# Performance work log

Measured on AMD Instinct MI355X. Metric: run time of the kernel, lower is better.

## Reference

```python
import jax, jax.numpy as jnp
import numpy as np

B, N, DEPTH = 64, 196, 6
EMBED = 384; CDIM = 384; DIM = EMBED + CDIM            # 768
HEADS = 8; DH = 64; INNER = HEADS * DH                 # 512
VD = INNER + CDIM; DV = VD // HEADS                    # 896, 112
SCALE = DH ** -0.5
EPS = 1e-5


def _bn(x, g, b):
    # BatchNorm1d in training mode applied to (b, e, n): per-channel stats over (b, n)
    m = x.mean(axis=(0, 1))
    v = x.var(axis=(0, 1))  # biased variance, as torch BN uses for normalization
    return (x - m) * jax.lax.rsqrt(v + EPS) * g + b


def setup_inputs() -> dict:
    key = jax.random.key(0)
    ks = jax.random.split(key, 8)
    s = 0.02
    d = {}
    d["x"] = jax.random.normal(ks[0], (B, N, DIM), jnp.float32)
    d["bn1_g"] = jnp.ones((DEPTH, DIM), jnp.float32)
    d["bn1_b"] = jnp.zeros((DEPTH, DIM), jnp.float32)
    d["Wqk"] = jax.random.normal(ks[1], (DEPTH, EMBED, 2 * INNER), jnp.float32) * s
    d["bqk"] = jnp.zeros((DEPTH, 2 * INNER), jnp.float32)
    d["Wv"] = jax.random.normal(ks[2], (DEPTH, DIM, VD), jnp.float32) * s
    d["bv"] = jnp.zeros((DEPTH, VD), jnp.float32)
    d["Wo"] = jax.random.normal(ks[3], (DEPTH, VD, DIM), jnp.float32) * s
    d["bo"] = jnp.zeros((DEPTH, DIM), jnp.float32)
    d["bn2_g"] = jnp.ones((DEPTH, DIM), jnp.float32)
    d["bn2_b"] = jnp.zeros((DEPTH, DIM), jnp.float32)
    d["W1"] = jax.random.normal(ks[4], (DEPTH, DIM, DIM), jnp.float32) * s
    d["b1"] = jnp.zeros((DEPTH, DIM), jnp.float32)
    d["bn3_g"] = jnp.ones((DEPTH, DIM), jnp.float32)
    d["bn3_b"] = jnp.zeros((DEPTH, DIM), jnp.float32)
    d["W2"] = jax.random.normal(ks[5], (DEPTH, DIM, DIM), jnp.float32) * s
    d["b2"] = jnp.zeros((DEPTH, DIM), jnp.float32)
    return d


def reference(x, bn1_g, bn1_b, Wqk, bqk, Wv, bv, Wo, bo,
              bn2_g, bn2_b, W1, b1, bn3_g, bn3_b, W2, b2):
    for i in range(DEPTH):
        # PreNorm(BatchNorm) + Attention + residual
        h = _bn(x, bn1_g[i], bn1_b[i])
        qk = h[:, :, -CDIM:] @ Wqk[i] + bqk[i]          # (B,N,2*INNER) from class slice
        q, k = jnp.split(qk, 2, axis=-1)
        v = h @ Wv[i] + bv[i]                            # (B,N,VD) from full dim
        q = q.reshape(B, N, HEADS, DH).transpose(0, 2, 1, 3)   # b h n d
        k = k.reshape(B, N, HEADS, DH).transpose(0, 2, 1, 3)
        v = v.reshape(B, N, HEADS, DV).transpose(0, 2, 1, 3)
        attn = jax.nn.softmax(jnp.einsum('bhnd,bhmd->bhnm', q, k) * SCALE, axis=-1)
        o = jnp.einsum('bhnm,bhmd->bhnd', attn, v)
        o = o.transpose(0, 2, 1, 3).reshape(B, N, VD)
        x = x + (o @ Wo[i] + bo[i])
        # PreNorm(BatchNorm) + FeedForward (Linear -> BN -> GELU -> Linear) + residual
        h = _bn(x, bn2_g[i], bn2_b[i])
        f = _bn(h @ W1[i] + b1[i], bn3_g[i], bn3_b[i])
        f = jax.nn.gelu(f, approximate=False)            # torch nn.GELU default (exact)
        x = x + (f @ W2[i] + b2[i])
    return x
```

## Files before the change

### kernel.cpp

```cpp
#include <hip/hip_runtime.h>
#include <hip/hip_bf16.h>
#include <stdint.h>


typedef __bf16 bf16x8 __attribute__((ext_vector_type(8)));
typedef __bf16 bf16x4 __attribute__((ext_vector_type(4)));
typedef float  f32x4  __attribute__((ext_vector_type(4)));

#define DIM_  768
#define SCALE_ 0.125f

__device__ __forceinline__ void gload16(const void* g, void* l) {
  __builtin_amdgcn_global_load_lds(
      (__attribute__((address_space(1))) void*)(g),
      (__attribute__((address_space(3))) void*)(l), 16, 0, 0);
}

__device__ __forceinline__ uint32_t cvt_pk_bf16(float lo, float hi) {
  uint32_t r;
  asm("v_cvt_pk_bf16_f32 %0, %1, %2" : "=v"(r) : "v"(lo), "v"(hi));
  return r;
}

__global__ void transpose_cvt(const float* __restrict__ W, __bf16* __restrict__ WT,
                              int K, int N) {
  __shared__ float t[32][33];
  const size_t zoff = (size_t)blockIdx.z * K * N;
  W  += zoff; WT += zoff;
  const int bx = blockIdx.x * 32;
  const int by = blockIdx.y * 32;
  for (int j = threadIdx.y; j < 32; j += 8)
    t[j][threadIdx.x] = W[(size_t)(by + j) * N + bx + threadIdx.x];
  __syncthreads();
  for (int j = threadIdx.y; j < 32; j += 8)
    WT[(size_t)(bx + j) * K + by + threadIdx.x] = (__bf16)t[threadIdx.x][j];
}

__global__ void cvt_bf16(const float* __restrict__ src, __bf16* __restrict__ dst) {
  const int i = blockIdx.x * 256 + threadIdx.x;
  f32x4 v = *(const f32x4*)(src + (size_t)i * 4);
  bf16x4 o;
  o[0] = (__bf16)v[0]; o[1] = (__bf16)v[1]; o[2] = (__bf16)v[2]; o[3] = (__bf16)v[3];
  *(bf16x4*)(dst + (size_t)i * 4) = o;
}

__global__ void bn_stats_part(const float* __restrict__ x, float* __restrict__ part) {
  const int col = blockIdx.x * 256 + threadIdx.x;
  const int r0  = blockIdx.y * 64;
  const float* p = x + (size_t)r0 * DIM_ + col;
  float s = 0.f, s2 = 0.f;
  for (int r = 0; r < 64; ++r) {
    float v = p[(size_t)r * DIM_];
    s += v; s2 += v * v;
  }
  float* q = part + ((size_t)blockIdx.y * DIM_ + col) * 2;
  q[0] = s; q[1] = s2;
}

__global__ void bn_stats_fin(const float* __restrict__ part, const float* __restrict__ g,
                             const float* __restrict__ b, float* __restrict__ sc) {
  const int col = blockIdx.x * 256 + threadIdx.x;
  float s = 0.f, s2 = 0.f;
  for (int p = 0; p < 196; ++p) {
    s  += part[((size_t)p * DIM_ + col) * 2];
    s2 += part[((size_t)p * DIM_ + col) * 2 + 1];
  }
  const float mean = s * (1.f / 12544.f);
  const float var  = s2 * (1.f / 12544.f) - mean * mean;
  const float rstd = rsqrtf(var + 1e-5f);
  const float scale = rstd * g[col];
  sc[col]        = scale;
  sc[DIM_ + col] = b[col] - mean * scale;
}

__global__ void bn_fin2(float* __restrict__ acc, const float* __restrict__ g,
                        const float* __restrict__ b, float* __restrict__ sc) {
  const int col = blockIdx.x * 256 + threadIdx.x;
  const float s  = acc[col * 2];
  const float s2 = acc[col * 2 + 1];
  acc[col * 2] = 0.f; acc[col * 2 + 1] = 0.f;
  const float mean = s * (1.f / 12544.f);
  const float var  = s2 * (1.f / 12544.f) - mean * mean;
  const float rstd = rsqrtf(var + 1e-5f);
  const float scale = rstd * g[col];
  sc[col]        = scale;
  sc[DIM_ + col] = b[col] - mean * scale;
}

__global__ void fold_attn(const __bf16* __restrict__ wqkT, const __bf16* __restrict__ wvT,
                          const float* __restrict__ bqk, const float* __restrict__ bv,
                          const float* __restrict__ sc,
                          __bf16* __restrict__ wqkT2, __bf16* __restrict__ wvT2,
                          float* __restrict__ bqk2, float* __restrict__ bv2) {
  const int b = blockIdx.x, tid = threadIdx.x;
  if (b < 192) {
    const int e = b * 2048 + tid * 8;
    const int k0 = e % 384;
    bf16x8 w = *(const bf16x8*)(wqkT + e);
    bf16x8 o;
#pragma unroll
    for (int j = 0; j < 8; ++j) o[j] = (__bf16)((float)w[j] * sc[384 + k0 + j]);
    *(bf16x8*)(wqkT2 + e) = o;
  } else if (b < 528) {
    const int e = (b - 192) * 2048 + tid * 8;
    const int k0 = e % 768;
    bf16x8 w = *(const bf16x8*)(wvT + e);
    bf16x8 o;
#pragma unroll
    for (int j = 0; j < 8; ++j) o[j] = (__bf16)((float)w[j] * sc[k0 + j]);
    *(bf16x8*)(wvT2 + e) = o;
  } else {
    const int lane = tid & 63, wv_ = tid >> 6;
    const int idx = (b - 528) * 4 + wv_;
    float acc = 0.f;
    if (idx < 1024) {
      for (int k = lane; k < 384; k += 64)
        acc += (float)wqkT[(size_t)idx * 384 + k] * sc[1152 + k];
#pragma unroll
      for (int off = 32; off; off >>= 1) acc += __shfl_xor(acc, off);
      if (lane == 0) bqk2[idx] = bqk[idx] + acc;
    } else {
      const int n2 = idx - 1024;
      for (int k = lane; k < 768; k += 64)
        acc += (float)wvT[(size_t)n2 * 768 + k] * sc[768 + k];
#pragma unroll
      for (int off = 32; off; off >>= 1) acc += __shfl_xor(acc, off);
      if (lane == 0) bv2[n2] = bv[n2] + acc;
    }
  }
}

__global__ void fold_ffn(const __bf16* __restrict__ w1T, const float* __restrict__ b1,
                         const float* __restrict__ sc,
                         __bf16* __restrict__ w1T2, float* __restrict__ b12) {
  const int b = blockIdx.x, tid = threadIdx.x;
  if (b < 288) {
    const int e = b * 2048 + tid * 8;
    const int k0 = e % 768;
    bf16x8 w = *(const bf16x8*)(w1T + e);
    bf16x8 o;
#pragma unroll
    for (int j = 0; j < 8; ++j) o[j] = (__bf16)((float)w[j] * sc[k0 + j]);
    *(bf16x8*)(w1T2 + e) = o;
  } else {
    const int lane = tid & 63, wv_ = tid >> 6;
    const int idx = (b - 288) * 4 + wv_;
    float acc = 0.f;
    for (int k = lane; k < 768; k += 64)
      acc += (float)w1T[(size_t)idx * 768 + k] * sc[768 + k];
#pragma unroll
    for (int off = 32; off; off >>= 1) acc += __shfl_xor(acc, off);
    if (lane == 0) b12[idx] = b1[idx] + acc;
  }
}

__global__ void bn_gelu_apply(const __bf16* __restrict__ f1, const float* __restrict__ sc,
                              __bf16* __restrict__ h) {
  const int i = blockIdx.x * 256 + threadIdx.x;
  const int c4 = i % 192;
  bf16x4 v4 = *(const bf16x4*)(f1 + (size_t)i * 4);
  f32x4 scl = *(const f32x4*)(sc + c4 * 4);
  f32x4 sh  = *(const f32x4*)(sc + DIM_ + c4 * 4);
  bf16x4 o;
#pragma unroll
  for (int j = 0; j < 4; ++j) {
    float y = (float)v4[j] * scl[j] + sh[j];
    float gl = 0.5f * y * (1.f + erff(y * 0.70710678118654752f));
    o[j] = (__bf16)gl;
  }
  *(bf16x4*)(h + (size_t)i * 4) = o;
}

template <int EPI, int STATS, int PANEL_X, int FINAL>
__global__ __launch_bounds__(256, 2) void gemm128(
    const __bf16* __restrict__ A, int lda,
    const __bf16* __restrict__ BT, int K,
    const float* __restrict__ bias,
    __bf16* outB, const __bf16* res16, float* __restrict__ outF, int ldc,
    float* __restrict__ statsAcc, int P, int S) {
  __shared__ __bf16 sA[128 * 64];
  __shared__ __bf16 sB[128 * 64];
  const int bid = blockIdx.x;
  const int xcd = bid & 7, r0b = bid >> 3;
  const int pl = r0b / S, sh = r0b - pl * S;
  const int p = pl * 8 + xcd;
  if (p >= P) return;
  const int mx = PANEL_X ? p : sh;
  const int ny = PANEL_X ? sh : p;

  const int tid = threadIdx.x;
  const int lane = tid & 63, wv = tid >> 6;
  const int l15 = lane & 15, hi = lane >> 4;
  const int m0 = mx * 128, n0 = ny * 128;
  const __bf16* Ab = A + (size_t)m0 * lda;
  const __bf16* Bb = BT + (size_t)n0 * K;
  const int wr = (wv >> 1) * 64, wc = (wv & 1) * 64;

  f32x4 acc[4][4] = {};

#define STAGE(kt)                                                             \
  {                                                                           \
    const int k0_ = (kt) << 6;                                                \
    _Pragma("unroll")                                                         \
    for (int i_ = 0; i_ < 4; ++i_) {                                          \
      const int o_ = i_ * 4096 + tid * 16;                                    \
      const int row_ = o_ >> 7;                                               \
      const int j_ = (o_ >> 4) & 7;                                           \
      const int src_ = (j_ ^ (row_ & 7)) << 3;                                \
      gload16(Ab + (size_t)row_ * lda + k0_ + src_,                           \
              &sA[i_ * 2048 + wv * 512]);                                     \
      gload16(Bb + (size_t)row_ * K + k0_ + src_,                             \
              &sB[i_ * 2048 + wv * 512]);                                     \
    }                                                                         \
  }

  const int nkt = K >> 6;
  for (int kt = 0; kt < nkt; ++kt) {
    if (kt) __syncthreads();
    STAGE(kt);
    asm volatile("s_waitcnt vmcnt(0)" ::: "memory");
    __syncthreads();
    const char* cA = (const char*)sA;
    const char* cB = (const char*)sB;
#pragma unroll
    for (int ks = 0; ks < 2; ++ks) {
      bf16x8 af[4], bfr[4];
#pragma unroll
      for (int m = 0; m < 4; ++m) {
        const int row = wr + m * 16 + l15;
        af[m] = *(const bf16x8*)(cA + row * 128 +
                                 ((ks * 64 + hi * 16) ^ ((row & 7) << 4)));
      }
#pragma unroll
      for (int n = 0; n < 4; ++n) {
        const int row = wc + n * 16 + l15;
        bfr[n] = *(const bf16x8*)(cB + row * 128 +
                                  ((ks * 64 + hi * 16) ^ ((row & 7) << 4)));
      }
#pragma unroll
      for (int m = 0; m < 4; ++m)
#pragma unroll
        for (int n = 0; n < 4; ++n)
          acc[m][n] = __builtin_amdgcn_mfma_f32_16x16x32_bf16(af[m], bfr[n], acc[m][n], 0, 0, 0);
    }
  }
#undef STAGE

  float* scol = (float*)sA;
  if (STATS) {
    __syncthreads();
    scol[tid] = 0.f;
    __syncthreads();
  }

  float cs[4], cs2[4];
  if (STATS)
#pragma unroll
    for (int n = 0; n < 4; ++n) { cs[n] = 0.f; cs2[n] = 0.f; }

#pragma unroll
  for (int m = 0; m < 4; ++m)
#pragma unroll
    for (int n = 0; n < 4; ++n) {
      const int cc = n0 + wc + n * 16 + l15;
      const float bc = (EPI == 2) ? 0.f : bias[cc];
      const int bbq = cc / 196, nn = cc - (cc / 196) * 196;
#pragma unroll
      for (int r = 0; r < 4; ++r) {
        const int rr = m0 + wr + m * 16 + hi * 4 + r;
        const float val = acc[m][n][r] + ((EPI == 2) ? bias[rr] : bc);
        float fv;
        if (EPI == 1) {
          const size_t idx = (size_t)rr * ldc + cc;
          fv = (float)res16[idx] + val;
          if (FINAL) outF[idx] = fv;
          else       outB[idx] = (__bf16)fv;
        } else if (EPI == 2) {
          fv = val;
          const int hq = rr / 112, dd = rr - (rr / 112) * 112;
          outB[((size_t)(bbq * 8 + hq) * 112 + dd) * 224 + nn] = (__bf16)fv;
        } else {
          fv = val;
          outB[(size_t)rr * ldc + cc] = (__bf16)fv;
        }
        if (STATS) { cs[n] += fv; cs2[n] += fv * fv; }
      }
    }

  if (STATS) {
#pragma unroll
    for (int n = 0; n < 4; ++n) {
      float s = cs[n], s2 = cs2[n];
      s += __shfl_xor(s, 16); s2 += __shfl_xor(s2, 16);
      s += __shfl_xor(s, 32); s2 += __shfl_xor(s2, 32);
      if (lane < 16) {
        atomicAdd(&scol[(wc + n * 16 + l15) * 2], s);
        atomicAdd(&scol[(wc + n * 16 + l15) * 2 + 1], s2);
      }
    }
    __syncthreads();
    if (tid < 128) {
      atomicAdd(&statsAcc[(size_t)(n0 + tid) * 2], scol[tid * 2]);
      atomicAdd(&statsAcc[(size_t)(n0 + tid) * 2 + 1], scol[tid * 2 + 1]);
    }
  }
}

#define SVOFF 25088
__global__ __launch_bounds__(512, 1) void attn_kernel(
    const __bf16* __restrict__ qk, const __bf16* __restrict__ vT,
    __bf16* __restrict__ og) {
  __shared__ __align__(16) char smem[75264];
  const int bid = blockIdx.x;
  const int half = bid >> 9, pairid = bid & 511;
  const int bb = pairid >> 3, hh = pairid & 7;
  const int tid = threadIdx.x, lane = tid & 63;
  const int wv = tid >> 6;
  const int l15 = lane & 15, hi = lane >> 4;

  const __bf16* qbase = qk + (size_t)bb * (196 * 1024) + hh * 64;
  const __bf16* kbase = qbase + 512;
  const __bf16* vbase = vT + (size_t)(bb * 8 + hh) * (112 * 224);
  __bf16* obase = og + (size_t)bb * (196 * 896) + hh * 112;

  char* sV = smem + SVOFF;

  for (int s = tid; s < 1568; s += 512) {
    const int n = s >> 3, j = s & 7;
    const int k8 = j ^ (n & 7);
    gload16(kbase + (size_t)n * 1024 + k8 * 8, smem + ((s >> 6) << 10));
  }
  for (int s = tid; s < 112 * 28; s += 512) {
    const int d = s / 28, j = s - d * 28;
    gload16(vbase + d * 224 + ((j ^ (d & 3)) << 3), sV + d * 448 + j * 16);
  }
  asm volatile("s_waitcnt vmcnt(0)" ::: "memory");
  __syncthreads();

  const int qt = half * 7 + wv;
  if (wv < 7 && qt < 13) {
    const int q0 = qt * 16;
    int qn = q0 + l15; if (qn > 195) qn = 195;
    const __bf16* qp = qbase + (size_t)qn * 1024 + hi * 8;
    const bf16x8 qa0 = *(const bf16x8*)(qp);
    const bf16x8 qa1 = *(const bf16x8*)(qp + 32);

    f32x4 s[13] = {};
#pragma unroll
    for (int nf = 0; nf < 13; ++nf) {
      int j = nf * 16 + l15; if (j > 195) j = 195;
      const int sw = (j & 7) << 4;
      const bf16x8 kb0 = *(const bf16x8*)(smem + j * 128 + ((hi * 16) ^ sw));
      const bf16x8 kb1 = *(const bf16x8*)(smem + j * 128 + ((64 + hi * 16) ^ sw));
      s[nf] = __builtin_amdgcn_mfma_f32_16x16x32_bf16(kb0, qa0, s[nf], 0, 0, 0);
      s[nf] = __builtin_amdgcn_mfma_f32_16x16x32_bf16(kb1, qa1, s[nf], 0, 0, 0);
    }

    float mx = -3.0e38f;
#pragma unroll
    for (int nf = 0; nf < 12; ++nf)
#pragma unroll
      for (int r = 0; r < 4; ++r) mx = fmaxf(mx, s[nf][r]);
    if (hi == 0)
#pragma unroll
      for (int r = 0; r < 4; ++r) mx = fmaxf(mx, s[12][r]);
    mx = fmaxf(mx, __shfl_xor(mx, 16));
    mx = fmaxf(mx, __shfl_xor(mx, 32));
    float sum = 0.f;
#pragma unroll
    for (int nf = 0; nf < 12; ++nf)
#pragma unroll
      for (int r = 0; r < 4; ++r) {
        const float pv = __expf((s[nf][r] - mx) * SCALE_);
        s[nf][r] = pv; sum += pv;
      }
#pragma unroll
    for (int r = 0; r < 4; ++r) {
      const float pv = (hi == 0) ? __expf((s[12][r] - mx) * SCALE_) : 0.f;
      s[12][r] = pv; sum += pv;
    }
    sum += __shfl_xor(sum, 16);
    sum += __shfl_xor(sum, 32);
    const float inv = 1.f / sum;
#pragma unroll
    for (int nf = 0; nf < 13; ++nf)
#pragma unroll
      for (int r = 0; r < 4; ++r) s[nf][r] *= inv;

    f32x4 oa[7] = {};
    const int sLo = l15 + ((hi & 1) << 5);
    const int sHi = sLo + 16;
    const bool up = (hi >> 1) != 0;
#pragma unroll
    for (int kk = 0; kk < 7; ++kk) {
      const uint32_t a0 = cvt_pk_bf16(s[2 * kk][0], s[2 * kk][1]);
      const uint32_t a1 = cvt_pk_bf16(s[2 * kk][2], s[2 * kk][3]);
      const uint32_t w0a = (uint32_t)__shfl((int)a0, sLo, 64);
      const uint32_t w1a = (uint32_t)__shfl((int)a1, sLo, 64);
      const uint32_t w2a = (uint32_t)__shfl((int)a0, sHi, 64);
      const uint32_t w3a = (uint32_t)__shfl((int)a1, sHi, 64);
      uint32_t w0, w1, w2, w3;
      if (kk < 6) {
        const uint32_t b0 = cvt_pk_bf16(s[2 * kk + 1][0], s[2 * kk + 1][1]);
        const uint32_t b1 = cvt_pk_bf16(s[2 * kk + 1][2], s[2 * kk + 1][3]);
        const uint32_t w0b = (uint32_t)__shfl((int)b0, sLo, 64);
        const uint32_t w1b = (uint32_t)__shfl((int)b1, sLo, 64);
        const uint32_t w2b = (uint32_t)__shfl((int)b0, sHi, 64);
        const uint32_t w3b = (uint32_t)__shfl((int)b1, sHi, 64);
        w0 = up ? w0b : w0a; w1 = up ? w1b : w1a;
        w2 = up ? w2b : w2a; w3 = up ? w3b : w3a;
      } else {
        w0 = up ? 0u : w0a; w1 = up ? 0u : w1a;
        w2 = up ? 0u : w2a; w3 = up ? 0u : w3a;
      }
      union { uint32_t u[4]; bf16x8 v; } pa;
      pa.u[0] = w0; pa.u[1] = w1; pa.u[2] = w2; pa.u[3] = w3;
#pragma unroll
      for (int nf = 0; nf < 7; ++nf) {
        const int d = nf * 16 + l15;
        const bf16x8 vbf = *(const bf16x8*)(sV + d * 448 +
                              ((kk * 64 + hi * 16) ^ ((d & 3) << 4)));
        oa[nf] = __builtin_amdgcn_mfma_f32_16x16x32_bf16(pa.v, vbf, oa[nf], 0, 0, 0);
      }
    }
#pragma unroll
    for (int nf = 0; nf < 7; ++nf)
#pragma unroll
      for (int r = 0; r < 4; ++r) {
        const int q = q0 + hi * 4 + r;
        if (q < 196) obase[(size_t)q * 896 + nf * 16 + l15] = (__bf16)oa[nf][r];
      }
  }
}

extern "C" void kernel_launch(void* const* d_in, const int* in_sizes, int n_in,
                              void* d_out, int out_size, void* d_ws, size_t ws_size,
                              hipStream_t stream) {
  (void)in_sizes; (void)n_in; (void)out_size; (void)ws_size;
  const float* x_in  = (const float*)d_in[0];
  const float* bn1_g = (const float*)d_in[1];
  const float* bn1_b = (const float*)d_in[2];
  const float* Wqk   = (const float*)d_in[3];
  const float* bqk   = (const float*)d_in[4];
  const float* Wv    = (const float*)d_in[5];
  const float* bv    = (const float*)d_in[6];
  const float* Wo    = (const float*)d_in[7];
  const float* bo    = (const float*)d_in[8];
  const float* bn2_g = (const float*)d_in[9];
  const float* bn2_b = (const float*)d_in[10];
  const float* W1    = (const float*)d_in[11];
  const float* b1    = (const float*)d_in[12];
  const float* bn3_g = (const float*)d_in[13];
  const float* bn3_b = (const float*)d_in[14];
  const float* W2    = (const float*)d_in[15];
  const float* b2    = (const float*)d_in[16];

  char* ws = (char*)d_ws;
  __bf16* vTb  = (__bf16*)(ws + 0);
  __bf16* wqkT = (__bf16*)(ws + 38535168);
  __bf16* wvT  = (__bf16*)(ws + 43253760);
  __bf16* woT  = (__bf16*)(ws + 51511296);
  __bf16* w1T  = (__bf16*)(ws + 59768832);
  __bf16* w2T  = (__bf16*)(ws + 66846720);
  __bf16* xb16 = (__bf16*)(ws + 73924608);
  __bf16* qkb  = (__bf16*)(ws + 93192192);
  __bf16* obuf = (__bf16*)(ws + 141361152);
  float*  part = (float*)(ws + 163840000);
  float*  sc   = (float*)(ws + 165044224);
  float*  sAcc = (float*)(ws + 165051392);
  __bf16* wqkT2= (__bf16*)(ws + 165057536);
  __bf16* wvT2 = (__bf16*)(ws + 165843968);
  __bf16* w1T2 = (__bf16*)(ws + 167220224);
  float*  bqk2 = (float*)(ws + 168399872);
  float*  bv2  = (float*)(ws + 168403968);
  float*  b12  = (float*)(ws + 168407552);
  __bf16* f1b  = qkb;
  __bf16* gout = obuf;

  const dim3 tb(256);
  const dim3 tb512(512);

  transpose_cvt<<<dim3(32, 12, 6), dim3(32, 8), 0, stream>>>(Wqk, wqkT, 384, 1024);
  transpose_cvt<<<dim3(28, 24, 6), dim3(32, 8), 0, stream>>>(Wv,  wvT,  768, 896);
  transpose_cvt<<<dim3(24, 28, 6), dim3(32, 8), 0, stream>>>(Wo,  woT,  896, 768);
  transpose_cvt<<<dim3(24, 24, 6), dim3(32, 8), 0, stream>>>(W1,  w1T,  768, 768);
  transpose_cvt<<<dim3(24, 24, 6), dim3(32, 8), 0, stream>>>(W2,  w2T,  768, 768);
  cvt_bf16<<<9408, tb, 0, stream>>>(x_in, xb16);
  hipMemsetAsync(sAcc, 0, 768 * 2 * sizeof(float), stream);
  hipMemsetAsync(vTb, 0, (size_t)512 * 112 * 224 * 2, stream);

  bn_stats_part<<<dim3(3, 196), tb, 0, stream>>>(x_in, part);
  bn_stats_fin<<<3, tb, 0, stream>>>(part, bn1_g, bn1_b, sc);

  const int gQK = 8 * 13 * 8;
  const int gV  = 8 * 13 * 7;
  const int gO  = 8 * 13 * 6;

  for (int i = 0; i < 6; ++i) {
    const __bf16* wqkT_i = wqkT + (size_t)i * 1024 * 384;
    const __bf16* wvT_i  = wvT  + (size_t)i * 896 * 768;
    const __bf16* woT_i  = woT  + (size_t)i * 768 * 896;
    const __bf16* w1T_i  = w1T  + (size_t)i * 768 * 768;
    const __bf16* w2T_i  = w2T  + (size_t)i * 768 * 768;

    fold_attn<<<1008, tb, 0, stream>>>(wqkT_i, wvT_i, bqk + i * 1024, bv + i * 896,
                                       sc, wqkT2, wvT2, bqk2, bv2);
    gemm128<0, 0, 1, 0><<<gQK, tb, 0, stream>>>(xb16 + 384, 768, wqkT2, 384,
                                                bqk2, qkb, nullptr, nullptr, 1024,
                                                nullptr, 98, 8);
    gemm128<2, 0, 0, 0><<<gV, tb, 0, stream>>>(wvT2, 768, xb16, 768,
                                               bv2, vTb, nullptr, nullptr, 12544,
                                               nullptr, 98, 7);
    attn_kernel<<<1024, tb512, 0, stream>>>(qkb, vTb, obuf);
    gemm128<1, 1, 1, 0><<<gO, tb, 0, stream>>>(obuf, 896, woT_i, 896,
                                               bo + i * 768, xb16, xb16, nullptr, 768,
                                               sAcc, 98, 6);

    bn_fin2<<<3, tb, 0, stream>>>(sAcc, bn2_g + i * 768, bn2_b + i * 768, sc);
    fold_ffn<<<480, tb, 0, stream>>>(w1T_i, b1 + i * 768, sc, w1T2, b12);
    gemm128<0, 1, 1, 0><<<gO, tb, 0, stream>>>(xb16, 768, w1T2, 768,
                                               b12, f1b, nullptr, nullptr, 768,
                                               sAcc, 98, 6);
    bn_fin2<<<3, tb, 0, stream>>>(sAcc, bn3_g + i * 768, bn3_b + i * 768, sc);
    bn_gelu_apply<<<9408, tb, 0, stream>>>(f1b, sc, gout);
    if (i < 5) {
      gemm128<1, 1, 1, 0><<<gO, tb, 0, stream>>>(gout, 768, w2T_i, 768,
                                                 b2 + i * 768, xb16, xb16, nullptr, 768,
                                                 sAcc, 98, 6);
      bn_fin2<<<3, tb, 0, stream>>>(sAcc, bn1_g + (i + 1) * 768, bn1_b + (i + 1) * 768, sc);
    } else {
      gemm128<1, 0, 1, 1><<<gO, tb, 0, stream>>>(gout, 768, w2T_i, 768,
                                                 b2 + i * 768, nullptr, xb16,
                                                 (float*)d_out, 768,
                                                 nullptr, 98, 6);
    }
  }
}
```

Before: 1.272 ms.

## Fuse QK and V projections into one GEMM with zero-padded QK weights

Merges the separate QK GEMM (K=384 on the class slice) and the transposed V GEMM into one launch over a concatenated 1920-column weight, with the QK weights zero-padded over the first 384 input channels. The epilogue routes columns below 1024 to the qk buffer and scatters the rest into the transposed per-head V layout, and the fold kernel builds the combined weight and bias. This removes one kernel launch and gives a larger, better-filled grid, but the QK half now does twice the MACs because of the zero padding, and V is written transposed with strided stores. The final FFN GEMM call is also passed a non-null residual pointer.

```diff
diff --git a/kernel.cpp b/kernel.cpp
--- a/kernel.cpp
+++ b/kernel.cpp
@@ -87,45 +87,44 @@
   sc[DIM_ + col] = b[col] - mean * scale;
 }
 
-__global__ void fold_attn(const __bf16* __restrict__ wqkT, const __bf16* __restrict__ wvT,
-                          const float* __restrict__ bqk, const float* __restrict__ bv,
-                          const float* __restrict__ sc,
-                          __bf16* __restrict__ wqkT2, __bf16* __restrict__ wvT2,
-                          float* __restrict__ bqk2, float* __restrict__ bv2) {
+__global__ void fold_qkv(const __bf16* __restrict__ wqkT, const __bf16* __restrict__ wvT,
+                         const float* __restrict__ bqk, const float* __restrict__ bv,
+                         const float* __restrict__ sc,
+                         __bf16* __restrict__ wqkv2, float* __restrict__ bqkv2) {
   const int b = blockIdx.x, tid = threadIdx.x;
-  if (b < 192) {
+  if (b < 720) {
     const int e = b * 2048 + tid * 8;
-    const int k0 = e % 384;
-    bf16x8 w = *(const bf16x8*)(wqkT + e);
-    bf16x8 o;
-#pragma unroll
-    for (int j = 0; j < 8; ++j) o[j] = (__bf16)((float)w[j] * sc[384 + k0 + j]);
-    *(bf16x8*)(wqkT2 + e) = o;
-  } else if (b < 528) {
-    const int e = (b - 192) * 2048 + tid * 8;
-    const int k0 = e % 768;
-    bf16x8 w = *(const bf16x8*)(wvT + e);
-    bf16x8 o;
-#pragma unroll
-    for (int j = 0; j < 8; ++j) o[j] = (__bf16)((float)w[j] * sc[k0 + j]);
-    *(bf16x8*)(wvT2 + e) = o;
+    const int n = e / 768, k0 = e - (e / 768) * 768;
+    bf16x8 o = {};
+    if (n < 1024) {
+      if (k0 >= 384) {
+        bf16x8 w = *(const bf16x8*)(wqkT + (size_t)n * 384 + (k0 - 384));
+#pragma unroll
+        for (int j = 0; j < 8; ++j) o[j] = (__bf16)((float)w[j] * sc[k0 + j]);
+      }
+    } else {
+      bf16x8 w = *(const bf16x8*)(wvT + (size_t)(n - 1024) * 768 + k0);
+#pragma unroll
+      for (int j = 0; j < 8; ++j) o[j] = (__bf16)((float)w[j] * sc[k0 + j]);
+    }
+    *(bf16x8*)(wqkv2 + e) = o;
   } else {
     const int lane = tid & 63, wv_ = tid >> 6;
-    const int idx = (b - 528) * 4 + wv_;
+    const int idx = (b - 720) * 4 + wv_;
     float acc = 0.f;
     if (idx < 1024) {
       for (int k = lane; k < 384; k += 64)
         acc += (float)wqkT[(size_t)idx * 384 + k] * sc[1152 + k];
 #pragma unroll
       for (int off = 32; off; off >>= 1) acc += __shfl_xor(acc, off);
-      if (lane == 0) bqk2[idx] = bqk[idx] + acc;
+      if (lane == 0) bqkv2[idx] = bqk[idx] + acc;
     } else {
       const int n2 = idx - 1024;
       for (int k = lane; k < 768; k += 64)
         acc += (float)wvT[(size_t)n2 * 768 + k] * sc[768 + k];
 #pragma unroll
       for (int off = 32; off; off >>= 1) acc += __shfl_xor(acc, off);
-      if (lane == 0) bv2[n2] = bv[n2] + acc;
+      if (lane == 0) bqkv2[idx] = bv[n2] + acc;
     }
   }
 }
@@ -263,22 +262,27 @@
 #pragma unroll
     for (int n = 0; n < 4; ++n) {
       const int cc = n0 + wc + n * 16 + l15;
-      const float bc = (EPI == 2) ? 0.f : bias[cc];
-      const int bbq = cc / 196, nn = cc - (cc / 196) * 196;
+      const float bc = bias[cc];
+      const int vd = cc - 1024;
+      const int hq = vd / 112, dd = vd - hq * 112;
 #pragma unroll
       for (int r = 0; r < 4; ++r) {
         const int rr = m0 + wr + m * 16 + hi * 4 + r;
-        const float val = acc[m][n][r] + ((EPI == 2) ? bias[rr] : bc);
+        const float val = acc[m][n][r] + bc;
         float fv;
         if (EPI == 1) {
           const size_t idx = (size_t)rr * ldc + cc;
           fv = (float)res16[idx] + val;
           if (FINAL) outF[idx] = fv;
           else       outB[idx] = (__bf16)fv;
-        } else if (EPI == 2) {
+        } else if (EPI == 3) {
           fv = val;
-          const int hq = rr / 112, dd = rr - (rr / 112) * 112;
-          outB[((size_t)(bbq * 8 + hq) * 112 + dd) * 224 + nn] = (__bf16)fv;
+          if (n0 < 1024) {
+            outB[(size_t)rr * 1024 + cc] = (__bf16)fv;
+          } else {
+            const int bbv = rr / 196, nn = rr - bbv * 196;
+            ((__bf16*)outF)[((size_t)(bbv * 8 + hq) * 112 + dd) * 224 + nn] = (__bf16)fv;
+          }
         } else {
           fv = val;
           outB[(size_t)rr * ldc + cc] = (__bf16)fv;
@@ -457,6 +461,10 @@
 
   char* ws = (char*)d_ws;
   __bf16* vTb  = (__bf16*)(ws + 0);
+  __bf16* wqkv2= (__bf16*)(ws + 25690112);
+  __bf16* w1T2 = (__bf16*)(ws + 28639232);
+  float*  bqkv2= (float*)(ws + 29818880);
+  float*  b12  = (float*)(ws + 29826560);
   __bf16* wqkT = (__bf16*)(ws + 38535168);
   __bf16* wvT  = (__bf16*)(ws + 43253760);
   __bf16* woT  = (__bf16*)(ws + 51511296);
@@ -468,12 +476,6 @@
   float*  part = (float*)(ws + 163840000);
   float*  sc   = (float*)(ws + 165044224);
   float*  sAcc = (float*)(ws + 165051392);
-  __bf16* wqkT2= (__bf16*)(ws + 165057536);
-  __bf16* wvT2 = (__bf16*)(ws + 165843968);
-  __bf16* w1T2 = (__bf16*)(ws + 167220224);
-  float*  bqk2 = (float*)(ws + 168399872);
-  float*  bv2  = (float*)(ws + 168403968);
-  float*  b12  = (float*)(ws + 168407552);
   __bf16* f1b  = qkb;
   __bf16* gout = obuf;
 
@@ -492,9 +494,8 @@
   bn_stats_part<<<dim3(3, 196), tb, 0, stream>>>(x_in, part);
   bn_stats_fin<<<3, tb, 0, stream>>>(part, bn1_g, bn1_b, sc);
 
-  const int gQK = 8 * 13 * 8;
-  const int gV  = 8 * 13 * 7;
-  const int gO  = 8 * 13 * 6;
+  const int gQKV = 8 * 13 * 15;
+  const int gO   = 8 * 13 * 6;
 
   for (int i = 0; i < 6; ++i) {
     const __bf16* wqkT_i = wqkT + (size_t)i * 1024 * 384;
@@ -503,14 +504,11 @@
     const __bf16* w1T_i  = w1T  + (size_t)i * 768 * 768;
     const __bf16* w2T_i  = w2T  + (size_t)i * 768 * 768;
 
-    fold_attn<<<1008, tb, 0, stream>>>(wqkT_i, wvT_i, bqk + i * 1024, bv + i * 896,
-                                       sc, wqkT2, wvT2, bqk2, bv2);
-    gemm128<0, 0, 1, 0><<<gQK, tb, 0, stream>>>(xb16 + 384, 768, wqkT2, 384,
-                                                bqk2, qkb, nullptr, nullptr, 1024,
-                                                nullptr, 98, 8);
-    gemm128<2, 0, 0, 0><<<gV, tb, 0, stream>>>(wvT2, 768, xb16, 768,
-                                               bv2, vTb, nullptr, nullptr, 12544,
-                                               nullptr, 98, 7);
+    fold_qkv<<<1200, tb, 0, stream>>>(wqkT_i, wvT_i, bqk + i * 1024, bv + i * 896,
+                                      sc, wqkv2, bqkv2);
+    gemm128<3, 0, 1, 0><<<gQKV, tb, 0, stream>>>(xb16, 768, wqkv2, 768,
+                                                 bqkv2, qkb, nullptr, (float*)vTb, 1024,
+                                                 nullptr, 98, 15);
     attn_kernel<<<1024, tb512, 0, stream>>>(qkb, vTb, obuf);
     gemm128<1, 1, 1, 0><<<gO, tb, 0, stream>>>(obuf, 896, woT_i, 896,
                                                bo + i * 768, xb16, xb16, nullptr, 768,
@@ -530,7 +528,7 @@
       bn_fin2<<<3, tb, 0, stream>>>(sAcc, bn1_g + (i + 1) * 768, bn1_b + (i + 1) * 768, sc);
     } else {
       gemm128<1, 0, 1, 1><<<gO, tb, 0, stream>>>(gout, 768, w2T_i, 768,
-                                                 b2 + i * 768, nullptr, xb16,
+                                                 b2 + i * 768, xb16, xb16,
                                                  (float*)d_out, 768,
                                                  nullptr, 98, 6);
     }
```

After: 1.421 ms (median of 2 runs). 1.12x slower.
